# Performance work log

Hardware: AMD Instinct MI355X
Metric: run time of the kernel (lower is better)

The kernel has to match this reference:

```python
import jax, jax.numpy as jnp
from jax import lax
import numpy as np

B, C, H, W = 8, 16, 128, 128
HID = 128


def setup_inputs() -> dict:
    key = jax.random.key(0)
    k1, k2, k3 = jax.random.split(key, 3)
    x = jax.random.uniform(k1, (B, C, H, W), dtype=jnp.float32)
    # fc1: Conv2d(3*C, HID, 1); fc2: Conv2d(HID, C, 1). Original zero-inits fc2;
    # we use small random weights so the dynamics (and grads) are non-trivial.
    w1 = jax.random.normal(k2, (HID, 3 * C), dtype=jnp.float32) * (1.0 / jnp.sqrt(3.0 * C))
    b1 = jnp.zeros((HID,), jnp.float32)
    w2 = jax.random.normal(k3, (C, HID), dtype=jnp.float32) * 0.02
    b2 = jnp.zeros((C,), jnp.float32)
    return {"x": x, "w1": w1, "b1": b1, "w2": w2, "b2": b2, "n_steps": 16}


def _dw_conv(x, k3x3):
    # depthwise 3x3 conv, same kernel for every channel, padding=1
    kern = jnp.broadcast_to(k3x3, (C, 1, 3, 3))
    return lax.conv_general_dilated(
        x, kern, window_strides=(1, 1), padding="SAME",
        feature_group_count=C,
        dimension_numbers=("NCHW", "OIHW", "NCHW"))


def _ca_step(out, step_key, w1, b1, w2, b2, sobel_x, sobel_y):
    sx = _dw_conv(out, sobel_x)
    sy = _dw_conv(out, sobel_y)
    ident = out  # identity 3x3 kernel == identity map
    perception = jnp.concatenate([ident, sx, sy], axis=1)  # [B,3C,H,W]
    h = jnp.einsum("bchw,oc->bohw", perception, w1) + b1[None, :, None, None]
    h = jax.nn.relu(h)
    diff = jnp.einsum("bchw,oc->bohw", h, w2) + b2[None, :, None, None]
    # stochastic per-pixel update mask, broadcast over channels
    mask = (jax.random.uniform(step_key, (B, 1, H, W)) < 0.5).astype(out.dtype)
    new = out + diff * mask
    # alive gate: 3x3 maxpool on alpha channel (index 3) > 0.1
    alpha = new[:, 3:4]
    pooled = lax.reduce_window(alpha, -jnp.inf, lax.max,
                               (1, 1, 3, 3), (1, 1, 1, 1), "SAME")
    alive = (pooled > 0.1).astype(new.dtype)
    return new * alive


def reference(x, w1, b1, w2, b2, n_steps):
    keys = jax.random.split(jax.random.key(42), n_steps)
    def body(out, k):
        return _ca_step(out, k, w1, b1, w2, b2, _SOBEL_X, _SOBEL_Y), None
    out, _ = lax.scan(body, x, keys)
    return out

_SOBEL_Y = jnp.array([[1.0, 2.0, 1.0], [0.0, 0.0, 0.0], [-1.0, -2.0, -1.0]],
                     dtype=jnp.float32) / 8.0
_SOBEL_X = _SOBEL_Y.T
```

## Files before the change

### kernel.cpp

```cpp
#include <hip/hip_runtime.h>
#include <stdint.h>

#define BB 8
#define CC 16
#define HH_ 128
#define WW 128
#define HIDN 128
#define HWSZ (HH_ * WW)
#define NPIX (BB * HWSZ)
#define NSTEPS 16

__host__ __device__ inline void threefry2x32(uint32_t k0, uint32_t k1,
                                             uint32_t x0, uint32_t x1,
                                             uint32_t* o0, uint32_t* o1) {
  uint32_t ks[3] = {k0, k1, k0 ^ k1 ^ 0x1BD11BDAu};
  const uint32_t rots[2][4] = {{13u, 15u, 26u, 6u}, {17u, 29u, 16u, 24u}};
  x0 += ks[0];
  x1 += ks[1];
#pragma unroll
  for (int g = 0; g < 5; ++g) {
    const uint32_t* r = rots[g & 1];
#pragma unroll
    for (int i = 0; i < 4; ++i) {
      x0 += x1;
      x1 = (x1 << r[i]) | (x1 >> (32u - r[i]));
      x1 ^= x0;
    }
    x0 += ks[(g + 1) % 3];
    x1 += ks[(g + 2) % 3] + (uint32_t)(g + 1);
  }
  *o0 = x0;
  *o1 = x1;
}

__device__ __forceinline__ float jax_mask_bit(uint32_t key0, uint32_t key1, int g) {
  uint32_t t0, t1;
  threefry2x32(key0, key1, 0u, (uint32_t)g, &t0, &t1);
  uint32_t bits = t0 ^ t1;
  float u = __uint_as_float((bits >> 9) | 0x3f800000u) - 1.0f;
  return (u < 0.5f) ? 1.0f : 0.0f;
}

__global__ __launch_bounds__(256, 2) void ca_step_mlp(
    const float* __restrict__ cur, const float* __restrict__ w1,
    const float* __restrict__ b1, const float* __restrict__ w2,
    const float* __restrict__ b2, float* __restrict__ nxt,
    uint32_t key0, uint32_t key1) {
  __shared__ float lw2t[HIDN * CC];

  for (int i = threadIdx.x; i < HIDN * CC; i += 256) {
    int o = i >> 7;
    int hh = i & (HIDN - 1);
    lw2t[hh * CC + o] = w2[i];
  }
  __syncthreads();

  const int g = blockIdx.x * 256 + threadIdx.x;
  const int b = g >> 14;
  const int hw = g & (HWSZ - 1);
  const int h = hw >> 7;
  const int w = hw & (WW - 1);

  const bool hu = h > 0, hd = h < HH_ - 1, wl = w > 0, wr = w < WW - 1;
  const int du = hu ? -WW : 0;
  const int dd = hd ? WW : 0;
  const int dl = wl ? -1 : 0;
  const int dr = wr ? 1 : 0;

  const float* xb = cur + (size_t)b * CC * HWSZ + hw;

  float p[48];
#pragma unroll
  for (int c = 0; c < CC; ++c) {
    const float* xc = xb + c * HWSZ;
    float n00 = xc[du + dl]; if (!(hu && wl)) n00 = 0.f;
    float n01 = xc[du];      if (!hu)         n01 = 0.f;
    float n02 = xc[du + dr]; if (!(hu && wr)) n02 = 0.f;
    float n10 = xc[dl];      if (!wl)         n10 = 0.f;
    float n11 = xc[0];
    float n12 = xc[dr];      if (!wr)         n12 = 0.f;
    float n20 = xc[dd + dl]; if (!(hd && wl)) n20 = 0.f;
    float n21 = xc[dd];      if (!hd)         n21 = 0.f;
    float n22 = xc[dd + dr]; if (!(hd && wr)) n22 = 0.f;
    p[c] = n11;
    p[16 + c] = (n00 - n02 + 2.f * (n10 - n12) + n20 - n22) * 0.125f;
    p[32 + c] = (n00 + 2.f * n01 + n02 - n20 - 2.f * n21 - n22) * 0.125f;
  }

  float diff[CC];
#pragma unroll
  for (int o = 0; o < CC; ++o) diff[o] = b2[o];

  for (int hh = 0; hh < HIDN; ++hh) {
    const float4* wrow = (const float4*)(w1 + hh * 48);
    float a0 = b1[hh], a1 = 0.f, a2 = 0.f, a3 = 0.f;
#pragma unroll
    for (int q = 0; q < 3; ++q) {
      float4 w0 = wrow[q * 4 + 0];
      float4 w1v = wrow[q * 4 + 1];
      float4 w2v = wrow[q * 4 + 2];
      float4 w3 = wrow[q * 4 + 3];
      const int base = q * 16;
      a0 = fmaf(w0.x, p[base + 0], a0);
      a0 = fmaf(w0.y, p[base + 1], a0);
      a0 = fmaf(w0.z, p[base + 2], a0);
      a0 = fmaf(w0.w, p[base + 3], a0);
      a1 = fmaf(w1v.x, p[base + 4], a1);
      a1 = fmaf(w1v.y, p[base + 5], a1);
      a1 = fmaf(w1v.z, p[base + 6], a1);
      a1 = fmaf(w1v.w, p[base + 7], a1);
      a2 = fmaf(w2v.x, p[base + 8], a2);
      a2 = fmaf(w2v.y, p[base + 9], a2);
      a2 = fmaf(w2v.z, p[base + 10], a2);
      a2 = fmaf(w2v.w, p[base + 11], a2);
      a3 = fmaf(w3.x, p[base + 12], a3);
      a3 = fmaf(w3.y, p[base + 13], a3);
      a3 = fmaf(w3.z, p[base + 14], a3);
      a3 = fmaf(w3.w, p[base + 15], a3);
    }
    float acc = (a0 + a1) + (a2 + a3);
    acc = fmaxf(acc, 0.f);
    const float4* w2row = (const float4*)(lw2t + hh * CC);
#pragma unroll
    for (int o4 = 0; o4 < 4; ++o4) {
      float4 wv = w2row[o4];
      diff[o4 * 4 + 0] = fmaf(wv.x, acc, diff[o4 * 4 + 0]);
      diff[o4 * 4 + 1] = fmaf(wv.y, acc, diff[o4 * 4 + 1]);
      diff[o4 * 4 + 2] = fmaf(wv.z, acc, diff[o4 * 4 + 2]);
      diff[o4 * 4 + 3] = fmaf(wv.w, acc, diff[o4 * 4 + 3]);
    }
  }

  const float m = jax_mask_bit(key0, key1, g);

  float* nb = nxt + (size_t)b * CC * HWSZ + hw;
#pragma unroll
  for (int c = 0; c < CC; ++c) {
    nb[c * HWSZ] = fmaf(diff[c], m, p[c]);
  }
}

__global__ __launch_bounds__(256) void ca_step_alive(
    const float* __restrict__ nw, float* __restrict__ out) {
  const int g = blockIdx.x * 256 + threadIdx.x;
  const int b = g >> 14;
  const int hw = g & (HWSZ - 1);
  const int h = hw >> 7;
  const int w = hw & (WW - 1);
  const bool hu = h > 0, hd = h < HH_ - 1, wl = w > 0, wr = w < WW - 1;

  const float* ab = nw + ((size_t)b * CC + 3) * HWSZ + hw;
  float pooled = ab[0];
  if (hu) {
    pooled = fmaxf(pooled, ab[-WW]);
    if (wl) pooled = fmaxf(pooled, ab[-WW - 1]);
    if (wr) pooled = fmaxf(pooled, ab[-WW + 1]);
  }
  if (hd) {
    pooled = fmaxf(pooled, ab[WW]);
    if (wl) pooled = fmaxf(pooled, ab[WW - 1]);
    if (wr) pooled = fmaxf(pooled, ab[WW + 1]);
  }
  if (wl) pooled = fmaxf(pooled, ab[-1]);
  if (wr) pooled = fmaxf(pooled, ab[1]);

  const float alive = (pooled > 0.1f) ? 1.0f : 0.0f;

  const float* nb = nw + (size_t)b * CC * HWSZ + hw;
  float* ob = out + (size_t)b * CC * HWSZ + hw;
#pragma unroll
  for (int c = 0; c < CC; ++c) ob[c * HWSZ] = nb[c * HWSZ] * alive;
}

extern "C" void kernel_launch(void* const* d_in, const int* in_sizes, int n_in,
                              void* d_out, int out_size, void* d_ws,
                              size_t ws_size, hipStream_t stream) {
  const float* x = (const float*)d_in[0];
  const float* w1 = (const float*)d_in[1];
  const float* b1 = (const float*)d_in[2];
  const float* w2 = (const float*)d_in[3];
  const float* b2 = (const float*)d_in[4];

  float* out = (float*)d_out;
  float* nbuf = (float*)d_ws;

  uint32_t k0s[NSTEPS], k1s[NSTEPS];
  for (int s = 0; s < NSTEPS; ++s)
    threefry2x32(0u, 42u, 0u, (uint32_t)s, &k0s[s], &k1s[s]);

  dim3 grid(NPIX / 256), block(256);
  for (int s = 0; s < NSTEPS; ++s) {
    const float* src = (s == 0) ? x : out;
    ca_step_mlp<<<grid, block, 0, stream>>>(src, w1, b1, w2, b2, nbuf,
                                            k0s[s], k1s[s]);
    ca_step_alive<<<grid, block, 0, stream>>>(nbuf, out);
  }
}
```

Baseline: 833.0 us.

## Process two rows per thread and stage w1/b1 in shared memory

Each thread of the MLP kernel now handles two vertically adjacent pixels. The 4x3 neighborhood loads are shared between them, and every w1/w2 weight fetch is reused for both pixels. The w1 and b1 weights are staged in LDS instead of being read from global or scalar memory inside the hidden loop. Blocks shrink to 128 threads with a launch bound of one block per SM. This roughly doubles register pressure per thread and halves the thread count, so occupancy could suffer.

```diff
diff --git a/kernel.cpp b/kernel.cpp
--- a/kernel.cpp
+++ b/kernel.cpp
@@ -41,102 +41,130 @@
   return (u < 0.5f) ? 1.0f : 0.0f;
 }
 
-__global__ __launch_bounds__(256, 2) void ca_step_mlp(
+__global__ __launch_bounds__(128, 1) void ca_step_mlp(
     const float* __restrict__ cur, const float* __restrict__ w1,
     const float* __restrict__ b1, const float* __restrict__ w2,
     const float* __restrict__ b2, float* __restrict__ nxt,
     uint32_t key0, uint32_t key1) {
+  __shared__ float lw1[HIDN * 48];
+  __shared__ float lb1[HIDN];
   __shared__ float lw2t[HIDN * CC];
 
-  for (int i = threadIdx.x; i < HIDN * CC; i += 256) {
-    int o = i >> 7;
-    int hh = i & (HIDN - 1);
-    lw2t[hh * CC + o] = w2[i];
+  {
+    const float4* gw1 = (const float4*)w1;
+    float4* s1 = (float4*)lw1;
+#pragma unroll
+    for (int i = threadIdx.x; i < HIDN * 12; i += 128) s1[i] = gw1[i];
+    lb1[threadIdx.x] = b1[threadIdx.x];
+    for (int i = threadIdx.x; i < HIDN * CC; i += 128) {
+      int hh = i >> 4, o = i & 15;
+      lw2t[i] = w2[o * HIDN + hh];
+    }
   }
   __syncthreads();
 
-  const int g = blockIdx.x * 256 + threadIdx.x;
-  const int b = g >> 14;
-  const int hw = g & (HWSZ - 1);
-  const int h = hw >> 7;
-  const int w = hw & (WW - 1);
-
-  const bool hu = h > 0, hd = h < HH_ - 1, wl = w > 0, wr = w < WW - 1;
+  const int g0 = blockIdx.x * 256 + threadIdx.x;
+  const int b = g0 >> 14;
+  const int hw0 = g0 & (HWSZ - 1);
+  const int r = hw0 >> 7;
+  const int w = hw0 & (WW - 1);
+
+  const bool hu = r > 0, hd = r < HH_ - 2, wl = w > 0, wr = w < WW - 1;
   const int du = hu ? -WW : 0;
-  const int dd = hd ? WW : 0;
+  const int dd = hd ? 2 * WW : 0;
   const int dl = wl ? -1 : 0;
   const int dr = wr ? 1 : 0;
 
-  const float* xb = cur + (size_t)b * CC * HWSZ + hw;
-
-  float p[48];
+  const float* xb = cur + (size_t)b * CC * HWSZ + hw0;
+
+  float p0[48], p1[48];
 #pragma unroll
   for (int c = 0; c < CC; ++c) {
     const float* xc = xb + c * HWSZ;
-    float n00 = xc[du + dl]; if (!(hu && wl)) n00 = 0.f;
-    float n01 = xc[du];      if (!hu)         n01 = 0.f;
-    float n02 = xc[du + dr]; if (!(hu && wr)) n02 = 0.f;
-    float n10 = xc[dl];      if (!wl)         n10 = 0.f;
-    float n11 = xc[0];
-    float n12 = xc[dr];      if (!wr)         n12 = 0.f;
-    float n20 = xc[dd + dl]; if (!(hd && wl)) n20 = 0.f;
-    float n21 = xc[dd];      if (!hd)         n21 = 0.f;
-    float n22 = xc[dd + dr]; if (!(hd && wr)) n22 = 0.f;
-    p[c] = n11;
-    p[16 + c] = (n00 - n02 + 2.f * (n10 - n12) + n20 - n22) * 0.125f;
-    p[32 + c] = (n00 + 2.f * n01 + n02 - n20 - 2.f * n21 - n22) * 0.125f;
-  }
-
-  float diff[CC];
-#pragma unroll
-  for (int o = 0; o < CC; ++o) diff[o] = b2[o];
+    float A0l = xc[du + dl], A0m = xc[du], A0r = xc[du + dr];
+    if (!hu) { A0l = 0.f; A0m = 0.f; A0r = 0.f; }
+    else { if (!wl) A0l = 0.f; if (!wr) A0r = 0.f; }
+    float A1l = xc[dl], A1m = xc[0], A1r = xc[dr];
+    if (!wl) A1l = 0.f;
+    if (!wr) A1r = 0.f;
+    float A2l = xc[WW + dl], A2m = xc[WW], A2r = xc[WW + dr];
+    if (!wl) A2l = 0.f;
+    if (!wr) A2r = 0.f;
+    float A3l = xc[dd + dl], A3m = xc[dd], A3r = xc[dd + dr];
+    if (!hd) { A3l = 0.f; A3m = 0.f; A3r = 0.f; }
+    else { if (!wl) A3l = 0.f; if (!wr) A3r = 0.f; }
+
+    p0[c] = A1m;
+    p0[16 + c] = (A0l - A0r + 2.f * (A1l - A1r) + A2l - A2r) * 0.125f;
+    p0[32 + c] = (A0l + 2.f * A0m + A0r - A2l - 2.f * A2m - A2r) * 0.125f;
+    p1[c] = A2m;
+    p1[16 + c] = (A1l - A1r + 2.f * (A2l - A2r) + A3l - A3r) * 0.125f;
+    p1[32 + c] = (A1l + 2.f * A1m + A1r - A3l - 2.f * A3m - A3r) * 0.125f;
+  }
+
+  float diff0[CC], diff1[CC];
+#pragma unroll
+  for (int o = 0; o < CC; ++o) {
+    float bo = b2[o];
+    diff0[o] = bo;
+    diff1[o] = bo;
+  }
 
   for (int hh = 0; hh < HIDN; ++hh) {
-    const float4* wrow = (const float4*)(w1 + hh * 48);
-    float a0 = b1[hh], a1 = 0.f, a2 = 0.f, a3 = 0.f;
-#pragma unroll
-    for (int q = 0; q < 3; ++q) {
-      float4 w0 = wrow[q * 4 + 0];
-      float4 w1v = wrow[q * 4 + 1];
-      float4 w2v = wrow[q * 4 + 2];
-      float4 w3 = wrow[q * 4 + 3];
-      const int base = q * 16;
-      a0 = fmaf(w0.x, p[base + 0], a0);
-      a0 = fmaf(w0.y, p[base + 1], a0);
-      a0 = fmaf(w0.z, p[base + 2], a0);
-      a0 = fmaf(w0.w, p[base + 3], a0);
-      a1 = fmaf(w1v.x, p[base + 4], a1);
-      a1 = fmaf(w1v.y, p[base + 5], a1);
-      a1 = fmaf(w1v.z, p[base + 6], a1);
-      a1 = fmaf(w1v.w, p[base + 7], a1);
-      a2 = fmaf(w2v.x, p[base + 8], a2);
-      a2 = fmaf(w2v.y, p[base + 9], a2);
-      a2 = fmaf(w2v.z, p[base + 10], a2);
-      a2 = fmaf(w2v.w, p[base + 11], a2);
-      a3 = fmaf(w3.x, p[base + 12], a3);
-      a3 = fmaf(w3.y, p[base + 13], a3);
-      a3 = fmaf(w3.z, p[base + 14], a3);
-      a3 = fmaf(w3.w, p[base + 15], a3);
-    }
-    float acc = (a0 + a1) + (a2 + a3);
-    acc = fmaxf(acc, 0.f);
-    const float4* w2row = (const float4*)(lw2t + hh * CC);
+    const float4* wrow = (const float4*)(lw1 + hh * 48);
+    const float bb = lb1[hh];
+    float a0 = bb, a1 = 0.f, a2 = 0.f, a3 = 0.f;
+    float c0 = bb, c1 = 0.f, c2 = 0.f, c3 = 0.f;
+#pragma unroll
+    for (int q = 0; q < 12; ++q) {
+      float4 wv = wrow[q];
+      const int k = q * 4;
+      float* ap;
+      float* cp;
+      switch (q & 3) {
+        case 0: ap = &a0; cp = &c0; break;
+        case 1: ap = &a1; cp = &c1; break;
+        case 2: ap = &a2; cp = &c2; break;
+        default: ap = &a3; cp = &c3; break;
+      }
+      float av = *ap, cv = *cp;
+      av = fmaf(wv.x, p0[k + 0], av);
+      av = fmaf(wv.y, p0[k + 1], av);
+      av = fmaf(wv.z, p0[k + 2], av);
+      av = fmaf(wv.w, p0[k + 3], av);
+      cv = fmaf(wv.x, p1[k + 0], cv);
+      cv = fmaf(wv.y, p1[k + 1], cv);
+      cv = fmaf(wv.z, p1[k + 2], cv);
+      cv = fmaf(wv.w, p1[k + 3], cv);
+      *ap = av;
+      *cp = cv;
+    }
+    float h0 = fmaxf((a0 + a1) + (a2 + a3), 0.f);
+    float h1 = fmaxf((c0 + c1) + (c2 + c3), 0.f);
+
+    const float4* w2r = (const float4*)(lw2t + hh * CC);
 #pragma unroll
     for (int o4 = 0; o4 < 4; ++o4) {
-      float4 wv = w2row[o4];
-      diff[o4 * 4 + 0] = fmaf(wv.x, acc, diff[o4 * 4 + 0]);
-      diff[o4 * 4 + 1] = fmaf(wv.y, acc, diff[o4 * 4 + 1]);
-      diff[o4 * 4 + 2] = fmaf(wv.z, acc, diff[o4 * 4 + 2]);
-      diff[o4 * 4 + 3] = fmaf(wv.w, acc, diff[o4 * 4 + 3]);
-    }
-  }
-
-  const float m = jax_mask_bit(key0, key1, g);
-
-  float* nb = nxt + (size_t)b * CC * HWSZ + hw;
+      float4 wv = w2r[o4];
+      diff0[o4 * 4 + 0] = fmaf(wv.x, h0, diff0[o4 * 4 + 0]);
+      diff0[o4 * 4 + 1] = fmaf(wv.y, h0, diff0[o4 * 4 + 1]);
+      diff0[o4 * 4 + 2] = fmaf(wv.z, h0, diff0[o4 * 4 + 2]);
+      diff0[o4 * 4 + 3] = fmaf(wv.w, h0, diff0[o4 * 4 + 3]);
+      diff1[o4 * 4 + 0] = fmaf(wv.x, h1, diff1[o4 * 4 + 0]);
+      diff1[o4 * 4 + 1] = fmaf(wv.y, h1, diff1[o4 * 4 + 1]);
+      diff1[o4 * 4 + 2] = fmaf(wv.z, h1, diff1[o4 * 4 + 2]);
+      diff1[o4 * 4 + 3] = fmaf(wv.w, h1, diff1[o4 * 4 + 3]);
+    }
+  }
+
+  const float m0 = jax_mask_bit(key0, key1, g0);
+  const float m1 = jax_mask_bit(key0, key1, g0 + 128);
+
+  float* nb = nxt + (size_t)b * CC * HWSZ + hw0;
 #pragma unroll
   for (int c = 0; c < CC; ++c) {
-    nb[c * HWSZ] = fmaf(diff[c], m, p[c]);
+    nb[c * HWSZ] = fmaf(diff0[c], m0, p0[c]);
+    nb[c * HWSZ + WW] = fmaf(diff1[c], m1, p1[c]);
   }
 }
 
@@ -188,11 +216,12 @@
   for (int s = 0; s < NSTEPS; ++s)
     threefry2x32(0u, 42u, 0u, (uint32_t)s, &k0s[s], &k1s[s]);
 
-  dim3 grid(NPIX / 256), block(256);
+  dim3 gridA(NPIX / 256), blockA(128);
+  dim3 gridB(NPIX / 256), blockB(256);
   for (int s = 0; s < NSTEPS; ++s) {
     const float* src = (s == 0) ? x : out;
-    ca_step_mlp<<<grid, block, 0, stream>>>(src, w1, b1, w2, b2, nbuf,
-                                            k0s[s], k1s[s]);
-    ca_step_alive<<<grid, block, 0, stream>>>(nbuf, out);
-  }
-}
+    ca_step_mlp<<<gridA, blockA, 0, stream>>>(src, w1, b1, w2, b2, nbuf,
+                                              k0s[s], k1s[s]);
+    ca_step_alive<<<gridB, blockB, 0, stream>>>(nbuf, out);
+  }
+}
```

Result: slower. 1.340 ms (+60.9%).
